# Performance work log

Hardware: AMD Instinct MI355X
Metric: run time of the kernel (lower is better)

Reference implementation:

```python
import jax, jax.numpy as jnp
import numpy as np

B, S, D = 4, 2048, 1024   # batch, seq_len, d_model
H, DK, DV = 16, 64, 64    # heads, key_size, head_size
NEG_BIG = 1e12


def setup_inputs() -> dict:
    key = jax.random.key(0)
    ks = jax.random.split(key, 11)
    s = 0.02  # weight scale
    return {
        "q": jax.random.normal(ks[0], (B, S, D), jnp.float32),
        "k": jax.random.normal(ks[1], (B, S, D), jnp.float32),
        "v": jax.random.normal(ks[2], (B, S, D), jnp.float32),
        "q_mask": jnp.ones((B, S), jnp.int32),
        "v_mask": jnp.ones((B, S), jnp.int32),
        "Wq": jax.random.normal(ks[3], (D, H * DK), jnp.float32) * s,
        "bq": jnp.zeros((H * DK,), jnp.float32),
        "Wk": jax.random.normal(ks[4], (D, H * DK), jnp.float32) * s,
        "bk": jnp.zeros((H * DK,), jnp.float32),
        "Wv": jax.random.normal(ks[5], (D, H * DV), jnp.float32) * s,
        "bv": jnp.zeros((H * DV,), jnp.float32),
        "Wo": jax.random.normal(ks[6], (H * DV, H * DV), jnp.float32) * s,
        "bo": jnp.zeros((H * DV,), jnp.float32),
    }


def reference(q, k, v, q_mask, v_mask, Wq, bq, Wk, bk, Wv, bv, Wo, bo):
    Bq, Sq, _ = q.shape
    Sk = k.shape[1]
    # projections -> (B, S, H, d)
    qw = (q @ Wq + bq).reshape(Bq, Sq, H, DK)
    kw = (k @ Wk + bk).reshape(Bq, Sk, H, DK)
    vw = (v @ Wv + bv).reshape(Bq, Sk, H, DV)
    # scores: (B, H, Sq, Sk)
    a = jnp.einsum('bjhd,bkhd->bhjk', qw, kw) / jnp.asarray(DK, qw.dtype) ** 0.5
    # v_mask: additive -inf-style masking on key axis (mode=1, axis=-1)
    vm = v_mask.astype(a.dtype)[:, None, None, :]
    a = a - (1.0 - vm) * NEG_BIG
    # a_mask = 'history_only' causal mask
    causal = jnp.tril(jnp.ones((Sq, Sk), a.dtype))
    a = a - (1.0 - causal) * NEG_BIG
    a = jax.nn.softmax(a, axis=-1)
    # attention output: (B, Sq, H, DV) -> (B, Sq, H*DV)
    o = jnp.einsum('bhjk,bkhd->bjhd', a, vw).reshape(Bq, Sq, H * DV)
    o = o @ Wo + bo
    # q_mask: multiplicative zeroing of padded query rows (mode=0)
    o = o * q_mask.astype(o.dtype)[:, :, None]
    return o
```

## Files before the change

### kernel.cpp

```cpp
#include <hip/hip_runtime.h>
#include <hip/hip_bf16.h>

#define Bb 4
#define Ss 2048
#define Dm 1024
#define Hh 16
#define DKk 64
#define DVv 64

using short8  = __attribute__((ext_vector_type(8))) short;
using short4v = __attribute__((ext_vector_type(4))) short;
using floatx4 = __attribute__((ext_vector_type(4))) float;

__device__ inline unsigned short f32_to_bf16(float f) {
    union { float f; unsigned int u; } x; x.f = f;
    unsigned int r = x.u + 0x7fffu + ((x.u >> 16) & 1u);
    return (unsigned short)(r >> 16);
}

__device__ inline unsigned int cvt_pk_bf16(float a, float b) {
    unsigned int r;
    asm("v_cvt_pk_bf16_f32 %0, %1, %2" : "=v"(r) : "v"(a), "v"(b));
    return r;
}

__device__ inline void dma16(const unsigned short* g, unsigned short* l) {
    __builtin_amdgcn_global_load_lds(
        (const __attribute__((address_space(1))) void*)g,
        (__attribute__((address_space(3))) void*)l, 16, 0, 0);
}

__global__ __launch_bounds__(256) void transpose_w4(
        const float* __restrict__ W0, const float* __restrict__ W1,
        const float* __restrict__ W2, const float* __restrict__ W3,
        unsigned short* __restrict__ T0, unsigned short* __restrict__ T1,
        unsigned short* __restrict__ T2, unsigned short* __restrict__ T3) {
    const float* W; unsigned short* Wt;
    switch (blockIdx.z) {
        case 0: W = W0; Wt = T0; break;
        case 1: W = W1; Wt = T1; break;
        case 2: W = W2; Wt = T2; break;
        default: W = W3; Wt = T3; break;
    }
    __shared__ float tile[32][33];
    int n0 = blockIdx.x * 32, k0 = blockIdx.y * 32;
    int tx = threadIdx.x, ty = threadIdx.y;
    #pragma unroll
    for (int i = 0; i < 32; i += 8)
        tile[ty + i][tx] = W[(size_t)(k0 + ty + i) * Dm + n0 + tx];
    __syncthreads();
    #pragma unroll
    for (int i = 0; i < 32; i += 8)
        Wt[(size_t)(n0 + ty + i) * Dm + k0 + tx] = f32_to_bf16(tile[tx][ty + i]);
}

__global__ __launch_bounds__(256) void cast_bf16(const float* __restrict__ X,
                                                 unsigned short* __restrict__ Y) {
    const int idx = blockIdx.x * 256 + threadIdx.x;
    const float4* x4 = (const float4*)X;
    float4 f0 = x4[idx * 2], f1 = x4[idx * 2 + 1];
    const float* p0 = (const float*)&f0;
    const float* p1 = (const float*)&f1;
    union { short8 v; unsigned short u[8]; } o;
    #pragma unroll
    for (int j = 0; j < 4; j++) {
        o.u[j]     = f32_to_bf16(p0[j]);
        o.u[4 + j] = f32_to_bf16(p1[j]);
    }
    *(short8*)(Y + (size_t)idx * 8) = o.v;
}

__global__ __launch_bounds__(256) void gemm_proj(const unsigned short* __restrict__ A,
                                                 const unsigned short* __restrict__ Bt,
                                                 const float* __restrict__ bias,
                                                 unsigned short* __restrict__ Out,
                                                 int mode) {
    const int wave = threadIdx.x >> 6;
    const int lane = threadIdx.x & 63;
    const int quad = lane >> 4;
    const int l16  = lane & 15;
    const int wr = wave & 1, wc = wave >> 1;
    const int m0 = blockIdx.x * 128;
    const int n0 = blockIdx.y * 128;

    __shared__ __align__(16) unsigned short Alds[4096];
    __shared__ __align__(16) unsigned short Blds[4096];

    const unsigned short* Asrc[2];
    const unsigned short* Bsrc[2];
    int Ldst[2];
    #pragma unroll
    for (int i = 0; i < 2; i++) {
        int L = (wave * 2 + i) * 64 + lane;
        int row = L >> 2, cpr = L & 3;
        int csrc = cpr ^ ((row >> 1) & 3);
        Ldst[i] = (wave * 2 + i) * 512;
        Asrc[i] = A  + (size_t)(m0 + row) * Dm + csrc * 8;
        Bsrc[i] = Bt + (size_t)(n0 + row) * Dm + csrc * 8;
    }

    int aoff[4], boff[4];
    #pragma unroll
    for (int r = 0; r < 4; r++) {
        int row = wr * 64 + r * 16 + l16;
        aoff[r] = row * 32 + (quad ^ ((row >> 1) & 3)) * 8;
        row = wc * 64 + r * 16 + l16;
        boff[r] = row * 32 + (quad ^ ((row >> 1) & 3)) * 8;
    }

    floatx4 acc[4][4] = {};

    for (int k0 = 0; k0 < Dm; k0 += 32) {
        __syncthreads();
        #pragma unroll
        for (int i = 0; i < 2; i++) {
            dma16(Asrc[i] + k0, &Alds[Ldst[i]]);
            dma16(Bsrc[i] + k0, &Blds[Ldst[i]]);
        }
        __syncthreads();

        short8 a[4], b[4];
        #pragma unroll
        for (int r = 0; r < 4; r++) a[r] = *(const short8*)(Alds + aoff[r]);
        #pragma unroll
        for (int c = 0; c < 4; c++) b[c] = *(const short8*)(Blds + boff[c]);
        #pragma unroll
        for (int r = 0; r < 4; r++)
            #pragma unroll
            for (int c = 0; c < 4; c++)
                acc[r][c] = __builtin_amdgcn_mfma_f32_16x16x32_bf16(a[r], b[c], acc[r][c], 0, 0, 0);
    }

    #pragma unroll
    for (int r = 0; r < 4; r++)
        #pragma unroll
        for (int c = 0; c < 4; c++) {
            int n = n0 + wc * 64 + c * 16 + l16;
            float bias_n = bias[n];
            int h = n >> 6, d = n & 63;
            #pragma unroll
            for (int i = 0; i < 4; i++) {
                int m = m0 + wr * 64 + r * 16 + quad * 4 + i;
                unsigned short ob = f32_to_bf16(acc[r][c][i] + bias_n);
                int bb = m >> 11, s = m & (Ss - 1);
                if (mode == 0)
                    Out[((size_t)(bb * Hh + h) * Ss + s) * 64 + d] = ob;
                else
                    Out[(((size_t)(bb * Hh + h) * 32 + (s >> 6)) * 64 + d) * 64 + (s & 63)] = ob;
            }
        }
}

__global__ __launch_bounds__(256) void gemm_final(const unsigned short* __restrict__ A,
                                                  const unsigned short* __restrict__ Bt,
                                                  const float* __restrict__ bias,
                                                  const int* __restrict__ q_mask,
                                                  float* __restrict__ Out) {
    const int wave = threadIdx.x >> 6;
    const int lane = threadIdx.x & 63;
    const int quad = lane >> 4;
    const int l16  = lane & 15;
    const int wr = wave & 1, wc = wave >> 1;
    const int m0 = blockIdx.x * 128;
    const int n0 = blockIdx.y * 128;

    __shared__ __align__(16) unsigned short Alds[4096];
    __shared__ __align__(16) unsigned short Blds[4096];

    const unsigned short* Asrc[2];
    const unsigned short* Bsrc[2];
    int Ldst[2];
    #pragma unroll
    for (int i = 0; i < 2; i++) {
        int L = (wave * 2 + i) * 64 + lane;
        int row = L >> 2, cpr = L & 3;
        int csrc = cpr ^ ((row >> 1) & 3);
        Ldst[i] = (wave * 2 + i) * 512;
        Asrc[i] = A  + (size_t)(m0 + row) * Dm + csrc * 8;
        Bsrc[i] = Bt + (size_t)(n0 + row) * Dm + csrc * 8;
    }

    int aoff[4], boff[4];
    #pragma unroll
    for (int r = 0; r < 4; r++) {
        int row = wr * 64 + r * 16 + l16;
        aoff[r] = row * 32 + (quad ^ ((row >> 1) & 3)) * 8;
        row = wc * 64 + r * 16 + l16;
        boff[r] = row * 32 + (quad ^ ((row >> 1) & 3)) * 8;
    }

    floatx4 acc[4][4] = {};

    for (int k0 = 0; k0 < Dm; k0 += 32) {
        __syncthreads();
        #pragma unroll
        for (int i = 0; i < 2; i++) {
            dma16(Asrc[i] + k0, &Alds[Ldst[i]]);
            dma16(Bsrc[i] + k0, &Blds[Ldst[i]]);
        }
        __syncthreads();

        short8 a[4], b[4];
        #pragma unroll
        for (int r = 0; r < 4; r++) a[r] = *(const short8*)(Alds + aoff[r]);
        #pragma unroll
        for (int c = 0; c < 4; c++) b[c] = *(const short8*)(Blds + boff[c]);
        #pragma unroll
        for (int r = 0; r < 4; r++)
            #pragma unroll
            for (int c = 0; c < 4; c++)
                acc[r][c] = __builtin_amdgcn_mfma_f32_16x16x32_bf16(a[r], b[c], acc[r][c], 0, 0, 0);
    }

    #pragma unroll
    for (int r = 0; r < 4; r++)
        #pragma unroll
        for (int c = 0; c < 4; c++) {
            int n = n0 + wc * 64 + c * 16 + l16;
            float bias_n = bias[n];
            #pragma unroll
            for (int i = 0; i < 4; i++) {
                int m = m0 + wr * 64 + r * 16 + quad * 4 + i;
                float qm = (float)q_mask[m];
                Out[(size_t)m * Dm + n] = (acc[r][c][i] + bias_n) * qm;
            }
        }
}

#define SCL 0.18033688f
#define PEN 1.44269504e12f

__global__ __launch_bounds__(256, 2) void attn_kernel(const unsigned short* __restrict__ Qp,
                                                      const unsigned short* __restrict__ Kp,
                                                      const unsigned short* __restrict__ Vt,
                                                      const int* __restrict__ v_mask,
                                                      unsigned short* __restrict__ AO) {
    const int tid  = threadIdx.x;
    const int wave = tid >> 6;
    const int lane = tid & 63;
    const int quad = lane >> 4;
    const int l16  = lane & 15;
    const int qp = blockIdx.x;
    const int h  = blockIdx.y;
    const int b  = blockIdx.z;
    const int bh = b * Hh + h;

    __shared__ __align__(16) unsigned short Klds[2][4096];
    __shared__ __align__(16) unsigned short Vlds[2][4096];
    __shared__ int allv[32];

    {
        const int tile = tid >> 3, sub = tid & 7;
        const int4 vmA = *(const int4*)(v_mask + b * Ss + tile * 64 + sub * 8);
        const int4 vmB = *(const int4*)(v_mask + b * Ss + tile * 64 + sub * 8 + 4);
        const bool ok = vmA.x && vmA.y && vmA.z && vmA.w &&
                        vmB.x && vmB.y && vmB.z && vmB.w;
        const unsigned long long bal = __ballot(ok);
        if (sub == 0)
            allv[tile] = (int)(((bal >> ((tile & 7) * 8)) & 0xFFull) == 0xFFull);
    }

    int srcOff[2], ldsDst[2];
    #pragma unroll
    for (int i = 0; i < 2; i++) {
        int G = i * 256 + tid;
        int grow = G >> 3, gc = G & 7;
        int fS = (grow & 3) | ((grow >> 1) & 4);
        srcOff[i] = grow * 64 + (gc ^ fS) * 8;
        ldsDst[i] = i * 2048 + wave * 512;
    }
    const unsigned short* Kt_base = Kp + (size_t)bh * Ss * 64;
    const unsigned short* Vt_base = Vt + (size_t)bh * 32 * 4096;
    const int* vm_base = v_mask + b * Ss;

    const int l3 = l16 & 3;
    const int fK = l3 | (((l16 >> 2) & 1) << 2);
    const int kslot = (quad ^ fK) * 8;
    int koff[4];
    #pragma unroll
    for (int kf = 0; kf < 4; kf++) {
        int row = (kf & 1) * 32 + ((l16 >> 2) << 3) + ((kf >> 1) << 2) + l3;
        koff[kf] = row * 64 + kslot;
    }
    const int fV = l3 | (((l16 >> 3) & 1) << 2);
    const int vslot = (quad ^ fV) * 8;
    int voff[4];
    #pragma unroll
    for (int f = 0; f < 4; f++) voff[f] = (f * 16 + l16) * 64 + vslot;

    short8 ones;
    #pragma unroll
    for (int i = 0; i < 8; i++) ones[i] = (short)0x3F80;

    const int kbq = quad * 8;

    auto run_phase = [&](int qi) {
        const int qbase = qi * 128 + wave * 32;
        const int q0 = qbase + l16;
        const unsigned short* qptr = Qp + ((size_t)bh * Ss + q0) * 64 + quad * 8;
        const short8 qf0 = *(const short8*)(qptr);
        const short8 qf1 = *(const short8*)(qptr + 32);
        const short8 qg0 = *(const short8*)(qptr + 16 * 64);
        const short8 qg1 = *(const short8*)(qptr + 16 * 64 + 32);

        floatx4 o0[4] = {}, o1[4] = {};
        floatx4 sm0 = {}, sm1 = {};

        const int diagw = 2 * qi + (wave >> 1);
        const int KT    = 2 * qi + 2;

        #pragma unroll
        for (int i = 0; i < 2; i++) {
            dma16(Kt_base + srcOff[i], &Klds[0][ldsDst[i]]);
            dma16(Vt_base + srcOff[i], &Vlds[0][ldsDst[i]]);
        }
        __syncthreads();

        int cur = 0;
        for (int kt = 0; kt < KT; kt++) {
            if (kt + 1 < KT) {
                const unsigned short* kn = Kt_base + (size_t)(kt + 1) * 4096;
                const unsigned short* vn = Vt_base + (size_t)(kt + 1) * 4096;
                #pragma unroll
                for (int i = 0; i < 2; i++) {
                    dma16(kn + srcOff[i], &Klds[cur ^ 1][ldsDst[i]]);
                    dma16(vn + srcOff[i], &Vlds[cur ^ 1][ldsDst[i]]);
                }
            }

            if (kt <= diagw) {
                const unsigned short* Kc = &Klds[cur][0];
                const unsigned short* Vc = &Vlds[cur][0];
                const int kk = kt * 64;

                floatx4 st0[4], st1[4];
                #pragma unroll
                for (int kf = 0; kf < 4; kf++) {
                    short8 a0 = *(const short8*)(Kc + koff[kf]);
                    short8 a1 = *(const short8*)(Kc + (koff[kf] ^ 32));
                    floatx4 t = {};
                    t = __builtin_amdgcn_mfma_f32_16x16x32_bf16(a0, qf0, t, 0, 0, 0);
                    t = __builtin_amdgcn_mfma_f32_16x16x32_bf16(a1, qf1, t, 0, 0, 0);
                    st0[kf] = t;
                    floatx4 u = {};
                    u = __builtin_amdgcn_mfma_f32_16x16x32_bf16(a0, qg0, u, 0, 0, 0);
                    u = __builtin_amdgcn_mfma_f32_16x16x32_bf16(a1, qg1, u, 0, 0, 0);
                    st1[kf] = u;
                }

                unsigned int pk0[4][2], pk1[4][2];
                if ((kt == diagw) || (!allv[kt])) {
                    #pragma unroll
                    for (int kf = 0; kf < 4; kf++) {
                        const int kb = kk + (kf & 1) * 32 + kbq + ((kf >> 1) << 2);
                        const int4 vm = *(const int4*)(vm_base + kb);
                        const int vmi[4] = {vm.x, vm.y, vm.z, vm.w};
                        float p0[4], p1[4];
                        #pragma unroll
                        for (int i = 0; i < 4; i++) {
                            const int key = kb + i;
                            const float penm = (vmi[i] == 0) ? PEN : 0.f;
                            const float pe0 = penm + ((key > q0) ? PEN : 0.f);
                            const float pe1 = penm + ((key > q0 + 16) ? PEN : 0.f);
                            p0[i] = exp2f(fmaf(st0[kf][i], SCL, -pe0));
                            p1[i] = exp2f(fmaf(st1[kf][i], SCL, -pe1));
                        }
                        pk0[kf][0] = cvt_pk_bf16(p0[0], p0[1]);
                        pk0[kf][1] = cvt_pk_bf16(p0[2], p0[3]);
                        pk1[kf][0] = cvt_pk_bf16(p1[0], p1[1]);
                        pk1[kf][1] = cvt_pk_bf16(p1[2], p1[3]);
                    }
                } else {
                    #pragma unroll
                    for (int kf = 0; kf < 4; kf++) {
                        float p0[4], p1[4];
                        #pragma unroll
                        for (int i = 0; i < 4; i++) {
                            p0[i] = exp2f(st0[kf][i] * SCL);
                            p1[i] = exp2f(st1[kf][i] * SCL);
                        }
                        pk0[kf][0] = cvt_pk_bf16(p0[0], p0[1]);
                        pk0[kf][1] = cvt_pk_bf16(p0[2], p0[3]);
                        pk1[kf][0] = cvt_pk_bf16(p1[0], p1[1]);
                        pk1[kf][1] = cvt_pk_bf16(p1[2], p1[3]);
                    }
                }

                union { short8 s; unsigned int u[4]; } pA0, pA1, pB0, pB1;
                pA0.u[0] = pk0[0][0]; pA0.u[1] = pk0[0][1];
                pA0.u[2] = pk0[2][0]; pA0.u[3] = pk0[2][1];
                pA1.u[0] = pk0[1][0]; pA1.u[1] = pk0[1][1];
                pA1.u[2] = pk0[3][0]; pA1.u[3] = pk0[3][1];
                pB0.u[0] = pk1[0][0]; pB0.u[1] = pk1[0][1];
                pB0.u[2] = pk1[2][0]; pB0.u[3] = pk1[2][1];
                pB1.u[0] = pk1[1][0]; pB1.u[1] = pk1[1][1];
                pB1.u[2] = pk1[3][0]; pB1.u[3] = pk1[3][1];

                sm0 = __builtin_amdgcn_mfma_f32_16x16x32_bf16(ones, pA0.s, sm0, 0, 0, 0);
                sm0 = __builtin_amdgcn_mfma_f32_16x16x32_bf16(ones, pA1.s, sm0, 0, 0, 0);
                sm1 = __builtin_amdgcn_mfma_f32_16x16x32_bf16(ones, pB0.s, sm1, 0, 0, 0);
                sm1 = __builtin_amdgcn_mfma_f32_16x16x32_bf16(ones, pB1.s, sm1, 0, 0, 0);

                #pragma unroll
                for (int f = 0; f < 4; f++) {
                    short8 v0 = *(const short8*)(Vc + voff[f]);
                    short8 v1 = *(const short8*)(Vc + (voff[f] ^ 32));
                    o0[f] = __builtin_amdgcn_mfma_f32_16x16x32_bf16(v0, pA0.s, o0[f], 0, 0, 0);
                    o0[f] = __builtin_amdgcn_mfma_f32_16x16x32_bf16(v1, pA1.s, o0[f], 0, 0, 0);
                    o1[f] = __builtin_amdgcn_mfma_f32_16x16x32_bf16(v0, pB0.s, o1[f], 0, 0, 0);
                    o1[f] = __builtin_amdgcn_mfma_f32_16x16x32_bf16(v1, pB1.s, o1[f], 0, 0, 0);
                }
            }

            __syncthreads();
            cur ^= 1;
        }

        const float ri0 = 1.0f / sm0[0];
        const float ri1 = 1.0f / sm1[0];
        unsigned short* aop0 = AO + ((size_t)b * Ss + q0) * (Hh * DVv) + h * 64 + quad * 4;
        unsigned short* aop1 = aop0 + (size_t)16 * (Hh * DVv);
        #pragma unroll
        for (int f = 0; f < 4; f++) {
            int2 w0, w1;
            w0.x = (int)cvt_pk_bf16(o0[f][0] * ri0, o0[f][1] * ri0);
            w0.y = (int)cvt_pk_bf16(o0[f][2] * ri0, o0[f][3] * ri0);
            *(int2*)(aop0 + f * 16) = w0;
            w1.x = (int)cvt_pk_bf16(o1[f][0] * ri1, o1[f][1] * ri1);
            w1.y = (int)cvt_pk_bf16(o1[f][2] * ri1, o1[f][3] * ri1);
            *(int2*)(aop1 + f * 16) = w1;
        }
    };

    run_phase(15 - qp);
    run_phase(qp);
}

extern "C" void kernel_launch(void* const* d_in, const int* in_sizes, int n_in,
                              void* d_out, int out_size, void* d_ws, size_t ws_size,
                              hipStream_t stream) {
    const float* q      = (const float*)d_in[0];
    const float* k      = (const float*)d_in[1];
    const float* v      = (const float*)d_in[2];
    const int*   q_mask = (const int*)d_in[3];
    const int*   v_mask = (const int*)d_in[4];
    const float* Wq     = (const float*)d_in[5];
    const float* bq     = (const float*)d_in[6];
    const float* Wk     = (const float*)d_in[7];
    const float* bk     = (const float*)d_in[8];
    const float* Wv     = (const float*)d_in[9];
    const float* bv     = (const float*)d_in[10];
    const float* Wo     = (const float*)d_in[11];
    const float* bo     = (const float*)d_in[12];
    float* out = (float*)d_out;

    char* ws = (char*)d_ws;
    const size_t WT_SZ = (size_t)Dm * Dm * 2;
    const size_t QP_SZ = (size_t)Bb * Hh * Ss * 64 * 2;
    unsigned short* Wtq = (unsigned short*)(ws);
    unsigned short* Wtk = (unsigned short*)(ws + WT_SZ);
    unsigned short* Wtv = (unsigned short*)(ws + 2 * WT_SZ);
    unsigned short* Wto = (unsigned short*)(ws + 3 * WT_SZ);
    unsigned short* Qp  = (unsigned short*)(ws + 4 * WT_SZ);
    unsigned short* Kp  = (unsigned short*)(ws + 4 * WT_SZ + QP_SZ);
    unsigned short* Vt  = (unsigned short*)(ws + 4 * WT_SZ + 2 * QP_SZ);
    unsigned short* AO  = (unsigned short*)(ws + 4 * WT_SZ + 3 * QP_SZ);

    hipLaunchKernelGGL(transpose_w4, dim3(Dm / 32, Dm / 32, 4), dim3(32, 8), 0, stream,
                       Wq, Wk, Wv, Wo, Wtq, Wtk, Wtv, Wto);

    const int M = Bb * Ss;
    const int castBlocks = M * Dm / (256 * 8);
    dim3 gg(M / 128, Dm / 128);

    hipLaunchKernelGGL(cast_bf16, dim3(castBlocks), dim3(256), 0, stream, q, AO);
    hipLaunchKernelGGL(gemm_proj, gg, dim3(256), 0, stream, AO, Wtq, bq, Qp, 0);
    hipLaunchKernelGGL(cast_bf16, dim3(castBlocks), dim3(256), 0, stream, k, AO);
    hipLaunchKernelGGL(gemm_proj, gg, dim3(256), 0, stream, AO, Wtk, bk, Kp, 0);
    hipLaunchKernelGGL(cast_bf16, dim3(castBlocks), dim3(256), 0, stream, v, AO);
    hipLaunchKernelGGL(gemm_proj, gg, dim3(256), 0, stream, AO, Wtv, bv, Vt, 1);

    dim3 ag(Ss / 256, Hh, Bb);
    hipLaunchKernelGGL(attn_kernel, ag, dim3(256), 0, stream, Qp, Kp, Vt, v_mask, AO);

    hipLaunchKernelGGL(gemm_final, gg, dim3(256), 0, stream, AO, Wto, bo, q_mask, out);
}
```

Baseline: 356.9 us.

## Fuse fp32-to-bf16 cast into batched QKV projection GEMM and reschedule attention blocks

The separate cast kernels are removed. The projection GEMM now loads fp32 activations into registers one k-step ahead, converts them with packed bf16 converts, and writes them to LDS itself. The three Q/K/V projections run as one launch indexed by blockIdx.z. The attention kernel changes from two causal phases per block to one 128-row query tile per block, using a flattened grid with an interleaved tile order to balance work across CUs. This drops the bf16 round trips and extra launches, but A-tile loads become plain register loads and stores rather than direct-to-LDS DMA, and the attention grid doubles in block count.

```diff
diff --git a/kernel.cpp b/kernel.cpp
--- a/kernel.cpp
+++ b/kernel.cpp
@@ -54,27 +54,22 @@
         Wt[(size_t)(n0 + ty + i) * Dm + k0 + tx] = f32_to_bf16(tile[tx][ty + i]);
 }
 
-__global__ __launch_bounds__(256) void cast_bf16(const float* __restrict__ X,
-                                                 unsigned short* __restrict__ Y) {
-    const int idx = blockIdx.x * 256 + threadIdx.x;
-    const float4* x4 = (const float4*)X;
-    float4 f0 = x4[idx * 2], f1 = x4[idx * 2 + 1];
-    const float* p0 = (const float*)&f0;
-    const float* p1 = (const float*)&f1;
-    union { short8 v; unsigned short u[8]; } o;
-    #pragma unroll
-    for (int j = 0; j < 4; j++) {
-        o.u[j]     = f32_to_bf16(p0[j]);
-        o.u[4 + j] = f32_to_bf16(p1[j]);
-    }
-    *(short8*)(Y + (size_t)idx * 8) = o.v;
-}
-
-__global__ __launch_bounds__(256) void gemm_proj(const unsigned short* __restrict__ A,
-                                                 const unsigned short* __restrict__ Bt,
-                                                 const float* __restrict__ bias,
-                                                 unsigned short* __restrict__ Out,
-                                                 int mode) {
+__global__ __launch_bounds__(256) void gemm_proj_f32(
+        const float* __restrict__ Aq, const float* __restrict__ Ak,
+        const float* __restrict__ Av,
+        const unsigned short* __restrict__ Btq, const unsigned short* __restrict__ Btk,
+        const unsigned short* __restrict__ Btv,
+        const float* __restrict__ bq, const float* __restrict__ bk,
+        const float* __restrict__ bv,
+        unsigned short* __restrict__ Oq, unsigned short* __restrict__ Ok,
+        unsigned short* __restrict__ Ov) {
+    const float* A; const unsigned short* Bt; const float* bias;
+    unsigned short* Out; int mode;
+    switch (blockIdx.z) {
+        case 0:  A = Aq; Bt = Btq; bias = bq; Out = Oq; mode = 0; break;
+        case 1:  A = Ak; Bt = Btk; bias = bk; Out = Ok; mode = 0; break;
+        default: A = Av; Bt = Btv; bias = bv; Out = Ov; mode = 1; break;
+    }
     const int wave = threadIdx.x >> 6;
     const int lane = threadIdx.x & 63;
     const int quad = lane >> 4;
@@ -86,15 +81,16 @@
     __shared__ __align__(16) unsigned short Alds[4096];
     __shared__ __align__(16) unsigned short Blds[4096];
 
-    const unsigned short* Asrc[2];
+    const float* Asrc[2];
     const unsigned short* Bsrc[2];
-    int Ldst[2];
+    int Ldst[2], Bdst[2];
     #pragma unroll
     for (int i = 0; i < 2; i++) {
         int L = (wave * 2 + i) * 64 + lane;
         int row = L >> 2, cpr = L & 3;
         int csrc = cpr ^ ((row >> 1) & 3);
-        Ldst[i] = (wave * 2 + i) * 512;
+        Ldst[i] = L * 8;
+        Bdst[i] = (wave * 2 + i) * 512;
         Asrc[i] = A  + (size_t)(m0 + row) * Dm + csrc * 8;
         Bsrc[i] = Bt + (size_t)(n0 + row) * Dm + csrc * 8;
     }
@@ -108,16 +104,36 @@
         boff[r] = row * 32 + (quad ^ ((row >> 1) & 3)) * 8;
     }
 
+    float4 ar[2][2];
+    #pragma unroll
+    for (int i = 0; i < 2; i++) {
+        ar[i][0] = *(const float4*)(Asrc[i]);
+        ar[i][1] = *(const float4*)(Asrc[i] + 4);
+    }
+
     floatx4 acc[4][4] = {};
 
     for (int k0 = 0; k0 < Dm; k0 += 32) {
         __syncthreads();
         #pragma unroll
         for (int i = 0; i < 2; i++) {
-            dma16(Asrc[i] + k0, &Alds[Ldst[i]]);
-            dma16(Bsrc[i] + k0, &Blds[Ldst[i]]);
+            union { short8 v; unsigned int u[4]; } w;
+            w.u[0] = cvt_pk_bf16(ar[i][0].x, ar[i][0].y);
+            w.u[1] = cvt_pk_bf16(ar[i][0].z, ar[i][0].w);
+            w.u[2] = cvt_pk_bf16(ar[i][1].x, ar[i][1].y);
+            w.u[3] = cvt_pk_bf16(ar[i][1].z, ar[i][1].w);
+            *(short8*)(Alds + Ldst[i]) = w.v;
+            dma16(Bsrc[i] + k0, &Blds[Bdst[i]]);
         }
         __syncthreads();
+
+        if (k0 + 32 < Dm) {
+            #pragma unroll
+            for (int i = 0; i < 2; i++) {
+                ar[i][0] = *(const float4*)(Asrc[i] + k0 + 32);
+                ar[i][1] = *(const float4*)(Asrc[i] + k0 + 36);
+            }
+        }
 
         short8 a[4], b[4];
         #pragma unroll
@@ -240,9 +256,19 @@
     const int lane = tid & 63;
     const int quad = lane >> 4;
     const int l16  = lane & 15;
-    const int qp = blockIdx.x;
-    const int h  = blockIdx.y;
-    const int b  = blockIdx.z;
+
+    const int n   = blockIdx.x;
+    const int hi4 = n >> 8, lo = n & 255;
+    const int t2  = (lo >> 6) & 3;
+    const int h   = (lo & 63) >> 2;
+    const int b   = lo & 3;
+    int qt;
+    switch (hi4) {
+        case 0:  qt = t2;      break;
+        case 1:  qt = 15 - t2; break;
+        case 2:  qt = 7 - t2;  break;
+        default: qt = 8 + t2;  break;
+    }
     const int bh = b * Hh + h;
 
     __shared__ __align__(16) unsigned short Klds[2][4096];
@@ -294,146 +320,141 @@
 
     const int kbq = quad * 8;
 
-    auto run_phase = [&](int qi) {
-        const int qbase = qi * 128 + wave * 32;
-        const int q0 = qbase + l16;
-        const unsigned short* qptr = Qp + ((size_t)bh * Ss + q0) * 64 + quad * 8;
-        const short8 qf0 = *(const short8*)(qptr);
-        const short8 qf1 = *(const short8*)(qptr + 32);
-        const short8 qg0 = *(const short8*)(qptr + 16 * 64);
-        const short8 qg1 = *(const short8*)(qptr + 16 * 64 + 32);
-
-        floatx4 o0[4] = {}, o1[4] = {};
-        floatx4 sm0 = {}, sm1 = {};
-
-        const int diagw = 2 * qi + (wave >> 1);
-        const int KT    = 2 * qi + 2;
-
-        #pragma unroll
-        for (int i = 0; i < 2; i++) {
-            dma16(Kt_base + srcOff[i], &Klds[0][ldsDst[i]]);
-            dma16(Vt_base + srcOff[i], &Vlds[0][ldsDst[i]]);
-        }
-        __syncthreads();
-
-        int cur = 0;
-        for (int kt = 0; kt < KT; kt++) {
-            if (kt + 1 < KT) {
-                const unsigned short* kn = Kt_base + (size_t)(kt + 1) * 4096;
-                const unsigned short* vn = Vt_base + (size_t)(kt + 1) * 4096;
-                #pragma unroll
-                for (int i = 0; i < 2; i++) {
-                    dma16(kn + srcOff[i], &Klds[cur ^ 1][ldsDst[i]]);
-                    dma16(vn + srcOff[i], &Vlds[cur ^ 1][ldsDst[i]]);
-                }
-            }
-
-            if (kt <= diagw) {
-                const unsigned short* Kc = &Klds[cur][0];
-                const unsigned short* Vc = &Vlds[cur][0];
-                const int kk = kt * 64;
-
-                floatx4 st0[4], st1[4];
+    const int qbase = qt * 128 + wave * 32;
+    const int q0 = qbase + l16;
+    const unsigned short* qptr = Qp + ((size_t)bh * Ss + q0) * 64 + quad * 8;
+    const short8 qf0 = *(const short8*)(qptr);
+    const short8 qf1 = *(const short8*)(qptr + 32);
+    const short8 qg0 = *(const short8*)(qptr + 16 * 64);
+    const short8 qg1 = *(const short8*)(qptr + 16 * 64 + 32);
+
+    floatx4 o0[4] = {}, o1[4] = {};
+    floatx4 sm0 = {}, sm1 = {};
+
+    const int diagw = 2 * qt + (wave >> 1);
+    const int KT    = 2 * qt + 2;
+
+    #pragma unroll
+    for (int i = 0; i < 2; i++) {
+        dma16(Kt_base + srcOff[i], &Klds[0][ldsDst[i]]);
+        dma16(Vt_base + srcOff[i], &Vlds[0][ldsDst[i]]);
+    }
+    __syncthreads();
+
+    int cur = 0;
+    for (int kt = 0; kt < KT; kt++) {
+        if (kt + 1 < KT) {
+            const unsigned short* kn = Kt_base + (size_t)(kt + 1) * 4096;
+            const unsigned short* vn = Vt_base + (size_t)(kt + 1) * 4096;
+            #pragma unroll
+            for (int i = 0; i < 2; i++) {
+                dma16(kn + srcOff[i], &Klds[cur ^ 1][ldsDst[i]]);
+                dma16(vn + srcOff[i], &Vlds[cur ^ 1][ldsDst[i]]);
+            }
+        }
+
+        if (kt <= diagw) {
+            const unsigned short* Kc = &Klds[cur][0];
+            const unsigned short* Vc = &Vlds[cur][0];
+            const int kk = kt * 64;
+
+            floatx4 st0[4], st1[4];
+            #pragma unroll
+            for (int kf = 0; kf < 4; kf++) {
+                short8 a0 = *(const short8*)(Kc + koff[kf]);
+                short8 a1 = *(const short8*)(Kc + (koff[kf] ^ 32));
+                floatx4 t = {};
+                t = __builtin_amdgcn_mfma_f32_16x16x32_bf16(a0, qf0, t, 0, 0, 0);
+                t = __builtin_amdgcn_mfma_f32_16x16x32_bf16(a1, qf1, t, 0, 0, 0);
+                st0[kf] = t;
+                floatx4 u = {};
+                u = __builtin_amdgcn_mfma_f32_16x16x32_bf16(a0, qg0, u, 0, 0, 0);
+                u = __builtin_amdgcn_mfma_f32_16x16x32_bf16(a1, qg1, u, 0, 0, 0);
+                st1[kf] = u;
+            }
+
+            unsigned int pk0[4][2], pk1[4][2];
+            if ((kt == diagw) || (!allv[kt])) {
                 #pragma unroll
                 for (int kf = 0; kf < 4; kf++) {
-                    short8 a0 = *(const short8*)(Kc + koff[kf]);
-                    short8 a1 = *(const short8*)(Kc + (koff[kf] ^ 32));
-                    floatx4 t = {};
-                    t = __builtin_amdgcn_mfma_f32_16x16x32_bf16(a0, qf0, t, 0, 0, 0);
-                    t = __builtin_amdgcn_mfma_f32_16x16x32_bf16(a1, qf1, t, 0, 0, 0);
-                    st0[kf] = t;
-                    floatx4 u = {};
-                    u = __builtin_amdgcn_mfma_f32_16x16x32_bf16(a0, qg0, u, 0, 0, 0);
-                    u = __builtin_amdgcn_mfma_f32_16x16x32_bf16(a1, qg1, u, 0, 0, 0);
-                    st1[kf] = u;
+                    const int kb = kk + (kf & 1) * 32 + kbq + ((kf >> 1) << 2);
+                    const int4 vm = *(const int4*)(vm_base + kb);
+                    const int vmi[4] = {vm.x, vm.y, vm.z, vm.w};
+                    float p0[4], p1[4];
+                    #pragma unroll
+                    for (int i = 0; i < 4; i++) {
+                        const int key = kb + i;
+                        const float penm = (vmi[i] == 0) ? PEN : 0.f;
+                        const float pe0 = penm + ((key > q0) ? PEN : 0.f);
+                        const float pe1 = penm + ((key > q0 + 16) ? PEN : 0.f);
+                        p0[i] = exp2f(fmaf(st0[kf][i], SCL, -pe0));
+                        p1[i] = exp2f(fmaf(st1[kf][i], SCL, -pe1));
+                    }
+                    pk0[kf][0] = cvt_pk_bf16(p0[0], p0[1]);
+                    pk0[kf][1] = cvt_pk_bf16(p0[2], p0[3]);
+                    pk1[kf][0] = cvt_pk_bf16(p1[0], p1[1]);
+                    pk1[kf][1] = cvt_pk_bf16(p1[2], p1[3]);
                 }
-
-                unsigned int pk0[4][2], pk1[4][2];
-                if ((kt == diagw) || (!allv[kt])) {
+            } else {
+                #pragma unroll
+                for (int kf = 0; kf < 4; kf++) {
+                    float p0[4], p1[4];
                     #pragma unroll
-                    for (int kf = 0; kf < 4; kf++) {
-                        const int kb = kk + (kf & 1) * 32 + kbq + ((kf >> 1) << 2);
-                        const int4 vm = *(const int4*)(vm_base + kb);
-                        const int vmi[4] = {vm.x, vm.y, vm.z, vm.w};
-                        float p0[4], p1[4];
-                        #pragma unroll
-                        for (int i = 0; i < 4; i++) {
-                            const int key = kb + i;
-                            const float penm = (vmi[i] == 0) ? PEN : 0.f;
-                            const float pe0 = penm + ((key > q0) ? PEN : 0.f);
-                            const float pe1 = penm + ((key > q0 + 16) ? PEN : 0.f);
-                            p0[i] = exp2f(fmaf(st0[kf][i], SCL, -pe0));
-                            p1[i] = exp2f(fmaf(st1[kf][i], SCL, -pe1));
-                        }
-                        pk0[kf][0] = cvt_pk_bf16(p0[0], p0[1]);
-                        pk0[kf][1] = cvt_pk_bf16(p0[2], p0[3]);
-                        pk1[kf][0] = cvt_pk_bf16(p1[0], p1[1]);
-                        pk1[kf][1] = cvt_pk_bf16(p1[2], p1[3]);
+                    for (int i = 0; i < 4; i++) {
+                        p0[i] = exp2f(st0[kf][i] * SCL);
+                        p1[i] = exp2f(st1[kf][i] * SCL);
                     }
-                } else {
-                    #pragma unroll
-                    for (int kf = 0; kf < 4; kf++) {
-                        float p0[4], p1[4];
-                        #pragma unroll
-                        for (int i = 0; i < 4; i++) {
-                            p0[i] = exp2f(st0[kf][i] * SCL);
-                            p1[i] = exp2f(st1[kf][i] * SCL);
-                        }
-                        pk0[kf][0] = cvt_pk_bf16(p0[0], p0[1]);
-                        pk0[kf][1] = cvt_pk_bf16(p0[2], p0[3]);
-                        pk1[kf][0] = cvt_pk_bf16(p1[0], p1[1]);
-                        pk1[kf][1] = cvt_pk_bf16(p1[2], p1[3]);
-                    }
+                    pk0[kf][0] = cvt_pk_bf16(p0[0], p0[1]);
+                    pk0[kf][1] = cvt_pk_bf16(p0[2], p0[3]);
+                    pk1[kf][0] = cvt_pk_bf16(p1[0], p1[1]);
+                    pk1[kf][1] = cvt_pk_bf16(p1[2], p1[3]);
                 }
-
-                union { short8 s; unsigned int u[4]; } pA0, pA1, pB0, pB1;
-                pA0.u[0] = pk0[0][0]; pA0.u[1] = pk0[0][1];
-                pA0.u[2] = pk0[2][0]; pA0.u[3] = pk0[2][1];
-                pA1.u[0] = pk0[1][0]; pA1.u[1] = pk0[1][1];
-                pA1.u[2] = pk0[3][0]; pA1.u[3] = pk0[3][1];
-                pB0.u[0] = pk1[0][0]; pB0.u[1] = pk1[0][1];
-                pB0.u[2] = pk1[2][0]; pB0.u[3] = pk1[2][1];
-                pB1.u[0] = pk1[1][0]; pB1.u[1] = pk1[1][1];
-                pB1.u[2] = pk1[3][0]; pB1.u[3] = pk1[3][1];
-
-                sm0 = __builtin_amdgcn_mfma_f32_16x16x32_bf16(ones, pA0.s, sm0, 0, 0, 0);
-                sm0 = __builtin_amdgcn_mfma_f32_16x16x32_bf16(ones, pA1.s, sm0, 0, 0, 0);
-                sm1 = __builtin_amdgcn_mfma_f32_16x16x32_bf16(ones, pB0.s, sm1, 0, 0, 0);
-                sm1 = __builtin_amdgcn_mfma_f32_16x16x32_bf16(ones, pB1.s, sm1, 0, 0, 0);
-
-                #pragma unroll
-                for (int f = 0; f < 4; f++) {
-                    short8 v0 = *(const short8*)(Vc + voff[f]);
-                    short8 v1 = *(const short8*)(Vc + (voff[f] ^ 32));
-                    o0[f] = __builtin_amdgcn_mfma_f32_16x16x32_bf16(v0, pA0.s, o0[f], 0, 0, 0);
-                    o0[f] = __builtin_amdgcn_mfma_f32_16x16x32_bf16(v1, pA1.s, o0[f], 0, 0, 0);
-                    o1[f] = __builtin_amdgcn_mfma_f32_16x16x32_bf16(v0, pB0.s, o1[f], 0, 0, 0);
-                    o1[f] = __builtin_amdgcn_mfma_f32_16x16x32_bf16(v1, pB1.s, o1[f], 0, 0, 0);
-                }
-            }
-
-            __syncthreads();
-            cur ^= 1;
-        }
-
-        const float ri0 = 1.0f / sm0[0];
-        const float ri1 = 1.0f / sm1[0];
-        unsigned short* aop0 = AO + ((size_t)b * Ss + q0) * (Hh * DVv) + h * 64 + quad * 4;
-        unsigned short* aop1 = aop0 + (size_t)16 * (Hh * DVv);
-        #pragma unroll
-        for (int f = 0; f < 4; f++) {
-            int2 w0, w1;
-            w0.x = (int)cvt_pk_bf16(o0[f][0] * ri0, o0[f][1] * ri0);
-            w0.y = (int)cvt_pk_bf16(o0[f][2] * ri0, o0[f][3] * ri0);
-            *(int2*)(aop0 + f * 16) = w0;
-            w1.x = (int)cvt_pk_bf16(o1[f][0] * ri1, o1[f][1] * ri1);
-            w1.y = (int)cvt_pk_bf16(o1[f][2] * ri1, o1[f][3] * ri1);
-            *(int2*)(aop1 + f * 16) = w1;
-        }
-    };
-
-    run_phase(15 - qp);
-    run_phase(qp);
+            }
+
+            union { short8 s; unsigned int u[4]; } pA0, pA1, pB0, pB1;
+            pA0.u[0] = pk0[0][0]; pA0.u[1] = pk0[0][1];
+            pA0.u[2] = pk0[2][0]; pA0.u[3] = pk0[2][1];
+            pA1.u[0] = pk0[1][0]; pA1.u[1] = pk0[1][1];
+            pA1.u[2] = pk0[3][0]; pA1.u[3] = pk0[3][1];
+            pB0.u[0] = pk1[0][0]; pB0.u[1] = pk1[0][1];
+            pB0.u[2] = pk1[2][0]; pB0.u[3] = pk1[2][1];
+            pB1.u[0] = pk1[1][0]; pB1.u[1] = pk1[1][1];
+            pB1.u[2] = pk1[3][0]; pB1.u[3] = pk1[3][1];
+
+            sm0 = __builtin_amdgcn_mfma_f32_16x16x32_bf16(ones, pA0.s, sm0, 0, 0, 0);
+            sm0 = __builtin_amdgcn_mfma_f32_16x16x32_bf16(ones, pA1.s, sm0, 0, 0, 0);
+            sm1 = __builtin_amdgcn_mfma_f32_16x16x32_bf16(ones, pB0.s, sm1, 0, 0, 0);
+            sm1 = __builtin_amdgcn_mfma_f32_16x16x32_bf16(ones, pB1.s, sm1, 0, 0, 0);
+
+            #pragma unroll
+            for (int f = 0; f < 4; f++) {
+                short8 v0 = *(const short8*)(Vc + voff[f]);
+                short8 v1 = *(const short8*)(Vc + (voff[f] ^ 32));
+                o0[f] = __builtin_amdgcn_mfma_f32_16x16x32_bf16(v0, pA0.s, o0[f], 0, 0, 0);
+                o0[f] = __builtin_amdgcn_mfma_f32_16x16x32_bf16(v1, pA1.s, o0[f], 0, 0, 0);
+                o1[f] = __builtin_amdgcn_mfma_f32_16x16x32_bf16(v0, pB0.s, o1[f], 0, 0, 0);
+                o1[f] = __builtin_amdgcn_mfma_f32_16x16x32_bf16(v1, pB1.s, o1[f], 0, 0, 0);
+            }
+        }
+
+        __syncthreads();
+        cur ^= 1;
+    }
+
+    const float ri0 = 1.0f / sm0[0];
+    const float ri1 = 1.0f / sm1[0];
+    unsigned short* aop0 = AO + ((size_t)b * Ss + q0) * (Hh * DVv) + h * 64 + quad * 4;
+    unsigned short* aop1 = aop0 + (size_t)16 * (Hh * DVv);
+    #pragma unroll
+    for (int f = 0; f < 4; f++) {
+        int2 w0, w1;
+        w0.x = (int)cvt_pk_bf16(o0[f][0] * ri0, o0[f][1] * ri0);
+        w0.y = (int)cvt_pk_bf16(o0[f][2] * ri0, o0[f][3] * ri0);
+        *(int2*)(aop0 + f * 16) = w0;
+        w1.x = (int)cvt_pk_bf16(o1[f][0] * ri1, o1[f][1] * ri1);
+        w1.y = (int)cvt_pk_bf16(o1[f][2] * ri1, o1[f][3] * ri1);
+        *(int2*)(aop1 + f * 16) = w1;
+    }
 }
 
 extern "C" void kernel_launch(void* const* d_in, const int* in_sizes, int n_in,
@@ -470,18 +491,13 @@
                        Wq, Wk, Wv, Wo, Wtq, Wtk, Wtv, Wto);
 
     const int M = Bb * Ss;
-    const int castBlocks = M * Dm / (256 * 8);
+    dim3 gp(M / 128, Dm / 128, 3);
+    hipLaunchKernelGGL(gemm_proj_f32, gp, dim3(256), 0, stream,
+                       q, k, v, Wtq, Wtk, Wtv, bq, bk, bv, Qp, Kp, Vt);
+
+    dim3 ag(Bb * Hh * (Ss / 128), 1, 1);
+    hipLaunchKernelGGL(attn_kernel, ag, dim3(256), 0, stream, Qp, Kp, Vt, v_mask, AO);
+
     dim3 gg(M / 128, Dm / 128);
-
-    hipLaunchKernelGGL(cast_bf16, dim3(castBlocks), dim3(256), 0, stream, q, AO);
-    hipLaunchKernelGGL(gemm_proj, gg, dim3(256), 0, stream, AO, Wtq, bq, Qp, 0);
-    hipLaunchKernelGGL(cast_bf16, dim3(castBlocks), dim3(256), 0, stream, k, AO);
-    hipLaunchKernelGGL(gemm_proj, gg, dim3(256), 0, stream, AO, Wtk, bk, Kp, 0);
-    hipLaunchKernelGGL(cast_bf16, dim3(castBlocks), dim3(256), 0, stream, v, AO);
-    hipLaunchKernelGGL(gemm_proj, gg, dim3(256), 0, stream, AO, Wtv, bv, Vt, 1);
-
-    dim3 ag(Ss / 256, Hh, Bb);
-    hipLaunchKernelGGL(attn_kernel, ag, dim3(256), 0, stream, Qp, Kp, Vt, v_mask, AO);
-
     hipLaunchKernelGGL(gemm_final, gg, dim3(256), 0, stream, AO, Wto, bo, q_mask, out);
 }
```

Measured after the change: 342.6 us. 4.0% less time.
